# Performance work log

Measured on AMD Instinct MI355X. Metric: run time of the kernel, lower is better.

Reference implementation:

```python
import jax, jax.numpy as jnp
import numpy as np

N_NODES = 250000
N_EDGES = 4000000

def gcn_layer(x, src, dst, W, b, n_nodes):
    # PyG GCNConv: linear transform, add self-loops, symmetric normalization,
    # scatter-add aggregation at target nodes, then bias.
    xw = x @ W                                            # [N, out]
    deg = jax.ops.segment_sum(jnp.ones_like(src, dtype=xw.dtype), dst,
                              num_segments=n_nodes) + 1.0  # +1 for self loop
    dinv = deg ** -0.5                                     # deg >= 1 due to self loops
    norm = dinv[src] * dinv[dst]                           # [E]
    agg = jax.ops.segment_sum(norm[:, None] * xw[src], dst,
                              num_segments=n_nodes)        # neighbor messages
    out = agg + (dinv * dinv)[:, None] * xw + b            # self-loop message + bias
    return out


def setup_inputs() -> dict:
    key = jax.random.key(0)
    ks = jax.random.split(key, 8)
    x = jax.random.normal(ks[0], (N_NODES, 2), dtype=jnp.float32)
    edge_index = jax.random.randint(ks[1], (2, N_EDGES), 0, N_NODES, dtype=jnp.int64)
    def glorot(k, shape):
        lim = np.sqrt(6.0 / (shape[0] + shape[1]))
        return jax.random.uniform(k, shape, jnp.float32, -lim, lim)
    return {
        "x": x,
        "edge_index": edge_index,
        "W1": glorot(ks[2], (2, 16)),  "b1": jnp.zeros((16,), jnp.float32),
        "W2": glorot(ks[3], (16, 16)), "b2": jnp.zeros((16,), jnp.float32),
        "W3": glorot(ks[4], (16, 1)),  "b3": jnp.zeros((1,), jnp.float32),
    }


def reference(x, edge_index, W1, b1, W2, b2, W3, b3):
    src, dst = edge_index[0], edge_index[1]
    n = x.shape[0]
    h = jax.nn.relu(gcn_layer(x, src, dst, W1, b1, n))
    h = jax.nn.relu(gcn_layer(h, src, dst, W2, b2, n))
    return gcn_layer(h, src, dst, W3, b3, n)
```

## Files before the change

### kernel.cpp

```cpp
#include <hip/hip_runtime.h>


constexpr int K   = 977;
constexpr int NPW = 256;
constexpr int G   = 256;
constexpr int F   = 16;


__global__ __launch_bounds__(1024) void k_bcount(const int* __restrict__ dst,
        int* __restrict__ bcount, int E, int chunk) {
    __shared__ int h[K];
    for (int k = threadIdx.x; k < K; k += 1024) h[k] = 0;
    __syncthreads();
    int beg = blockIdx.x * chunk;
    int end = min(beg + chunk, E);
    for (int i = beg + threadIdx.x; i < end; i += 1024) {
        int d = __builtin_nontemporal_load(&dst[i]);
        atomicAdd(&h[d >> 8], 1);
    }
    __syncthreads();
    for (int k = threadIdx.x; k < K; k += 1024)
        bcount[blockIdx.x * K + k] = h[k];
}

__global__ __launch_bounds__(1024) void k_scan(int* __restrict__ bcount,
        int* __restrict__ colbase, int E) {
    __shared__ int tot[1024];
    int k = threadIdx.x;
    int s = 0;
    if (k < K) for (int b = 0; b < G; ++b) s += bcount[b * K + k];
    tot[k] = s;
    __syncthreads();
    for (int off = 1; off < 1024; off <<= 1) {
        int t = (k >= off) ? tot[k - off] : 0;
        __syncthreads();
        tot[k] += t;
        __syncthreads();
    }
    if (k < K) {
        int run = tot[k] - s;
        colbase[k] = run;
        for (int b = 0; b < G; ++b) {
            int t = bcount[b * K + k];
            bcount[b * K + k] = run;
            run += t;
        }
    }
    if (k == 0) colbase[K] = E;
}

__global__ __launch_bounds__(1024) void k_bfill(const int* __restrict__ src,
        const int* __restrict__ dst, const int* __restrict__ base,
        int* __restrict__ ent, int E, int chunk) {
    __shared__ int cur[K];
    for (int k = threadIdx.x; k < K; k += 1024)
        cur[k] = base[blockIdx.x * K + k];
    __syncthreads();
    int beg = blockIdx.x * chunk;
    int end = min(beg + chunk, E);
    for (int i = beg + threadIdx.x; i < end; i += 1024) {
        int d = __builtin_nontemporal_load(&dst[i]);
        int s = __builtin_nontemporal_load(&src[i]);
        int pos = atomicAdd(&cur[d >> 8], 1);
        ent[pos] = (s << 8) | (d & 255);
    }
}


__global__ __launch_bounds__(256) void k_prep(const int* __restrict__ ent,
        const int* __restrict__ colbase, const float* __restrict__ x,
        float* __restrict__ dinv, float* __restrict__ dx, int n) {
    __shared__ int h[NPW];
    h[threadIdx.x] = 0;
    __syncthreads();
    int beg = colbase[blockIdx.x], end = colbase[blockIdx.x + 1];
    for (int e = beg + threadIdx.x; e < end; e += 256) {
        int v = __builtin_nontemporal_load(&ent[e]);
        atomicAdd(&h[v & 255], 1);
    }
    __syncthreads();
    int i = (blockIdx.x << 8) + threadIdx.x;
    if (i < n) {
        float di = rsqrtf((float)h[threadIdx.x] + 1.0f);
        dinv[i] = di;
        float2 xv = reinterpret_cast<const float2*>(x)[i];
        reinterpret_cast<float2*>(dx)[i] = make_float2(di * xv.x, di * xv.y);
    }
}


__global__ __launch_bounds__(512) void k_layer1(const int* __restrict__ ent,
        const int* __restrict__ colbase, const float* __restrict__ dinv,
        const float* __restrict__ dx, const float* __restrict__ W1,
        const float* __restrict__ b1, float* __restrict__ dh1, int n) {
    __shared__ float acc[NPW * 2];
    __shared__ float sW[32];
    __shared__ float sb[16];
    if (threadIdx.x < 32) sW[threadIdx.x] = W1[threadIdx.x];
    if (threadIdx.x >= 32 && threadIdx.x < 48) sb[threadIdx.x - 32] = b1[threadIdx.x - 32];
    for (int t = threadIdx.x; t < NPW * 2; t += 512) acc[t] = 0.0f;
    __syncthreads();
    int beg = colbase[blockIdx.x], end = colbase[blockIdx.x + 1];
    int e = beg + threadIdx.x;
    for (; e + 512 < end; e += 1024) {
        int v0 = __builtin_nontemporal_load(&ent[e]);
        int v1 = __builtin_nontemporal_load(&ent[e + 512]);
        float2 a0 = reinterpret_cast<const float2*>(dx)[v0 >> 8];
        float2 a1 = reinterpret_cast<const float2*>(dx)[v1 >> 8];
        atomicAdd(&acc[(v0 & 255) * 2 + 0], a0.x);
        atomicAdd(&acc[(v0 & 255) * 2 + 1], a0.y);
        atomicAdd(&acc[(v1 & 255) * 2 + 0], a1.x);
        atomicAdd(&acc[(v1 & 255) * 2 + 1], a1.y);
    }
    if (e < end) {
        int v = __builtin_nontemporal_load(&ent[e]);
        float2 a = reinterpret_cast<const float2*>(dx)[v >> 8];
        atomicAdd(&acc[(v & 255) * 2 + 0], a.x);
        atomicAdd(&acc[(v & 255) * 2 + 1], a.y);
    }
    __syncthreads();
    int r = threadIdx.x;
    if (r < NPW) {
        int i = (blockIdx.x << 8) + r;
        if (i < n) {
            float di = dinv[i];
            float2 ds = reinterpret_cast<const float2*>(dx)[i];
            float a0 = di * (acc[r * 2 + 0] + ds.x);
            float a1 = di * (acc[r * 2 + 1] + ds.y);
            float4* orow = reinterpret_cast<float4*>(dh1 + (size_t)i * F);
#pragma unroll
            for (int q = 0; q < 4; ++q) {
                float4 o;
                o.x = di * fmaxf(a0 * sW[4*q+0] + a1 * sW[16 + 4*q+0] + sb[4*q+0], 0.0f);
                o.y = di * fmaxf(a0 * sW[4*q+1] + a1 * sW[16 + 4*q+1] + sb[4*q+1], 0.0f);
                o.z = di * fmaxf(a0 * sW[4*q+2] + a1 * sW[16 + 4*q+2] + sb[4*q+2], 0.0f);
                o.w = di * fmaxf(a0 * sW[4*q+3] + a1 * sW[16 + 4*q+3] + sb[4*q+3], 0.0f);
                orow[q] = o;
            }
        }
    }
}


__global__ __launch_bounds__(512) void k_layer2(const int* __restrict__ ent,
        const int* __restrict__ colbase, const float* __restrict__ dinv,
        const float* __restrict__ dh1, const float* __restrict__ W2,
        const float* __restrict__ b2, const float* __restrict__ W3,
        float* __restrict__ dxw3, int n) {
    __shared__ float acc[NPW * 17];
    __shared__ float sW2[256];
    __shared__ float sW3[16];
    __shared__ float sb[16];
    if (threadIdx.x < 256) sW2[threadIdx.x] = W2[threadIdx.x];
    if (threadIdx.x >= 256 && threadIdx.x < 272) sW3[threadIdx.x - 256] = W3[threadIdx.x - 256];
    if (threadIdx.x >= 272 && threadIdx.x < 288) sb[threadIdx.x - 272] = b2[threadIdx.x - 272];
    for (int t = threadIdx.x; t < NPW * 17; t += 512) acc[t] = 0.0f;
    __syncthreads();
    int beg = colbase[blockIdx.x], end = colbase[blockIdx.x + 1];
    int q4 = (threadIdx.x & 3) * 4;
    int eg = threadIdx.x >> 2;
    int e = beg + eg;
    for (; e + 128 < end; e += 256) {
        int v0 = __builtin_nontemporal_load(&ent[e]);
        int v1 = __builtin_nontemporal_load(&ent[e + 128]);
        float4 r0 = *reinterpret_cast<const float4*>(dh1 + (size_t)(v0 >> 8) * F + q4);
        float4 r1 = *reinterpret_cast<const float4*>(dh1 + (size_t)(v1 >> 8) * F + q4);
        int b0 = (v0 & 255) * 17 + q4;
        int b1_ = (v1 & 255) * 17 + q4;
        atomicAdd(&acc[b0 + 0], r0.x);
        atomicAdd(&acc[b0 + 1], r0.y);
        atomicAdd(&acc[b0 + 2], r0.z);
        atomicAdd(&acc[b0 + 3], r0.w);
        atomicAdd(&acc[b1_ + 0], r1.x);
        atomicAdd(&acc[b1_ + 1], r1.y);
        atomicAdd(&acc[b1_ + 2], r1.z);
        atomicAdd(&acc[b1_ + 3], r1.w);
    }
    if (e < end) {
        int v = __builtin_nontemporal_load(&ent[e]);
        float4 r = *reinterpret_cast<const float4*>(dh1 + (size_t)(v >> 8) * F + q4);
        int b0 = (v & 255) * 17 + q4;
        atomicAdd(&acc[b0 + 0], r.x);
        atomicAdd(&acc[b0 + 1], r.y);
        atomicAdd(&acc[b0 + 2], r.z);
        atomicAdd(&acc[b0 + 3], r.w);
    }
    __syncthreads();
    int r = threadIdx.x;
    if (r < NPW) {
        int i = (blockIdx.x << 8) + r;
        if (i < n) {
            float di = dinv[i];
            const float* dh = dh1 + (size_t)i * F;
            float a[16];
#pragma unroll
            for (int q = 0; q < 16; ++q) a[q] = di * (acc[r * 17 + q] + dh[q]);
            float sum = 0.0f;
#pragma unroll
            for (int c = 0; c < 16; ++c) {
                float h = sb[c];
#pragma unroll
                for (int q = 0; q < 16; ++q) h += a[q] * sW2[q * 16 + c];
                sum += fmaxf(h, 0.0f) * sW3[c];
            }
            dxw3[i] = di * sum;
        }
    }
}


__global__ __launch_bounds__(512) void k_out(const int* __restrict__ ent,
        const int* __restrict__ colbase, const float* __restrict__ dinv,
        const float* __restrict__ dxw3, const float* __restrict__ b3,
        float* __restrict__ out, int n) {
    __shared__ float acc[NPW];
    for (int t = threadIdx.x; t < NPW; t += 512) acc[t] = 0.0f;
    __syncthreads();
    int beg = colbase[blockIdx.x], end = colbase[blockIdx.x + 1];
    int e = beg + threadIdx.x;
    for (; e + 512 < end; e += 1024) {
        int v0 = __builtin_nontemporal_load(&ent[e]);
        int v1 = __builtin_nontemporal_load(&ent[e + 512]);
        float s0 = dxw3[v0 >> 8];
        float s1 = dxw3[v1 >> 8];
        atomicAdd(&acc[v0 & 255], s0);
        atomicAdd(&acc[v1 & 255], s1);
    }
    if (e < end) {
        int v = __builtin_nontemporal_load(&ent[e]);
        atomicAdd(&acc[v & 255], dxw3[v >> 8]);
    }
    __syncthreads();
    int r = threadIdx.x;
    if (r < NPW) {
        int i = (blockIdx.x << 8) + r;
        if (i < n) out[i] = dinv[i] * (acc[r] + dxw3[i]) + b3[0];
    }
}


extern "C" void kernel_launch(void* const* d_in, const int* in_sizes, int n_in,
                              void* d_out, int out_size, void* d_ws, size_t ws_size,
                              hipStream_t stream) {
    const float* x  = (const float*)d_in[0];
    const int*   ei = (const int*)d_in[1];
    const float* W1 = (const float*)d_in[2];
    const float* b1 = (const float*)d_in[3];
    const float* W2 = (const float*)d_in[4];
    const float* b2 = (const float*)d_in[5];
    const float* W3 = (const float*)d_in[6];
    const float* b3 = (const float*)d_in[7];

    const int n = in_sizes[0] / 2;
    const int E = in_sizes[1] / 2;
    const int* src = ei;
    const int* dst = ei + E;

    char* w = (char*)d_ws;
    int*   ent     = (int*)w;                    w += (size_t)E * 4;
    int*   bcount  = (int*)w;                    w += (size_t)G * K * 4;
    float* dinv    = (float*)w;                  w += (size_t)n * 4;
    float* dx      = (float*)w;                  w += (size_t)n * 2 * 4;
    float* dh1     = (float*)w;                  w += (size_t)n * F * 4;
    float* dxw3    = (float*)w;                  w += (size_t)n * 4;
    int*   colbase = (int*)w;                    w += (size_t)(K + 1) * 4;
    float* out     = (float*)d_out;

    const int chunk = (E + G - 1) / G;

    k_bcount<<<G, 1024, 0, stream>>>(dst, bcount, E, chunk);
    k_scan  <<<1, 1024, 0, stream>>>(bcount, colbase, E);
    k_bfill <<<G, 1024, 0, stream>>>(src, dst, bcount, ent, E, chunk);

    k_prep<<<K, 256, 0, stream>>>(ent, colbase, x, dinv, dx, n);

    k_layer1<<<K, 512, 0, stream>>>(ent, colbase, dinv, dx, W1, b1, dh1, n);
    k_layer2<<<K, 512, 0, stream>>>(ent, colbase, dinv, dh1, W2, b2, W3, dxw3, n);
    k_out   <<<K, 512, 0, stream>>>(ent, colbase, dinv, dxw3, b3, out, n);
}
```

Before: 544.1 us.

## Pre-sort edges by source tile before destination bucketing; retune layer2 block size

Adds a first counting-sort pass that groups edges by source-node tile (8192 nodes), packing dst and the source offset into one word held in a buffer aliased over the node-feature pool. The destination bucket fill then runs over source-ordered edges, so within each destination bucket the source ids come out roughly sorted. The aim is better cache locality for the dh1/dx gathers in the layer kernels. This costs an extra full pass over the edge list plus scan kernels. Layer2 separately drops to 256 threads with a 4-way unrolled gather loop.

```diff
diff --git a/kernel.cpp b/kernel.cpp
--- a/kernel.cpp
+++ b/kernel.cpp
@@ -1,13 +1,74 @@
 #include <hip/hip_runtime.h>
 
 
-constexpr int K   = 977;
-constexpr int NPW = 256;
-constexpr int G   = 256;
-constexpr int F   = 16;
-
-
-__global__ __launch_bounds__(1024) void k_bcount(const int* __restrict__ dst,
+constexpr int K    = 977;
+constexpr int NPW  = 256;
+constexpr int G    = 256;
+constexpr int F    = 16;
+constexpr int TILE = 8192;
+constexpr int TMAX = 64;
+
+
+__global__ __launch_bounds__(1024) void k_acount(const int* __restrict__ src,
+        int* __restrict__ acount, int E, int chunk, int T) {
+    __shared__ int h[TMAX];
+    if (threadIdx.x < TMAX) h[threadIdx.x] = 0;
+    __syncthreads();
+    int beg = blockIdx.x * chunk;
+    int end = min(beg + chunk, E);
+    for (int i = beg + threadIdx.x; i < end; i += 1024) {
+        int s = __builtin_nontemporal_load(&src[i]);
+        atomicAdd(&h[s / TILE], 1);
+    }
+    __syncthreads();
+    if (threadIdx.x < T) acount[blockIdx.x * T + threadIdx.x] = h[threadIdx.x];
+}
+
+__global__ __launch_bounds__(256) void k_ascan(int* __restrict__ acount,
+        int* __restrict__ tbase, int E, int T) {
+    __shared__ int tot[TMAX];
+    int t = threadIdx.x;
+    if (t < T) {
+        int s = 0;
+        for (int b = 0; b < G; ++b) s += acount[b * T + t];
+        tot[t] = s;
+    }
+    __syncthreads();
+    if (t == 0) {
+        int run = 0;
+        for (int q = 0; q < T; ++q) { int c = tot[q]; tot[q] = run; run += c; }
+    }
+    __syncthreads();
+    if (t < T) {
+        int run = tot[t];
+        tbase[t] = run;
+        for (int b = 0; b < G; ++b) {
+            int c = acount[b * T + t];
+            acount[b * T + t] = run;
+            run += c;
+        }
+    }
+    if (t == 0) tbase[T] = E;
+}
+
+__global__ __launch_bounds__(1024) void k_afill(const int* __restrict__ src,
+        const int* __restrict__ dst, const int* __restrict__ abase,
+        unsigned int* __restrict__ entA, int E, int chunk, int T) {
+    __shared__ int cur[TMAX];
+    if (threadIdx.x < T) cur[threadIdx.x] = abase[blockIdx.x * T + threadIdx.x];
+    __syncthreads();
+    int beg = blockIdx.x * chunk;
+    int end = min(beg + chunk, E);
+    for (int i = beg + threadIdx.x; i < end; i += 1024) {
+        int s = __builtin_nontemporal_load(&src[i]);
+        int d = __builtin_nontemporal_load(&dst[i]);
+        int pos = atomicAdd(&cur[s / TILE], 1);
+        entA[pos] = ((unsigned int)d << 13) | (unsigned int)(s & (TILE - 1));
+    }
+}
+
+
+__global__ __launch_bounds__(1024) void k_bcount(const unsigned int* __restrict__ entA,
         int* __restrict__ bcount, int E, int chunk) {
     __shared__ int h[K];
     for (int k = threadIdx.x; k < K; k += 1024) h[k] = 0;
@@ -15,8 +76,8 @@
     int beg = blockIdx.x * chunk;
     int end = min(beg + chunk, E);
     for (int i = beg + threadIdx.x; i < end; i += 1024) {
-        int d = __builtin_nontemporal_load(&dst[i]);
-        atomicAdd(&h[d >> 8], 1);
+        unsigned int v = __builtin_nontemporal_load(&entA[i]);
+        atomicAdd(&h[(v >> 13) >> 8], 1);
     }
     __syncthreads();
     for (int k = threadIdx.x; k < K; k += 1024)
@@ -49,18 +110,23 @@
     if (k == 0) colbase[K] = E;
 }
 
-__global__ __launch_bounds__(1024) void k_bfill(const int* __restrict__ src,
-        const int* __restrict__ dst, const int* __restrict__ base,
-        int* __restrict__ ent, int E, int chunk) {
+__global__ __launch_bounds__(1024) void k_bfill(const unsigned int* __restrict__ entA,
+        const int* __restrict__ tbase, const int* __restrict__ base,
+        int* __restrict__ ent, int E, int chunk, int T) {
     __shared__ int cur[K];
+    __shared__ int tb[TMAX + 1];
     for (int k = threadIdx.x; k < K; k += 1024)
         cur[k] = base[blockIdx.x * K + k];
+    if (threadIdx.x <= T) tb[threadIdx.x] = tbase[threadIdx.x];
     __syncthreads();
     int beg = blockIdx.x * chunk;
     int end = min(beg + chunk, E);
+    int t = 0;
     for (int i = beg + threadIdx.x; i < end; i += 1024) {
-        int d = __builtin_nontemporal_load(&dst[i]);
-        int s = __builtin_nontemporal_load(&src[i]);
+        while (i >= tb[t + 1]) ++t;
+        unsigned int v = __builtin_nontemporal_load(&entA[i]);
+        int d = (int)(v >> 13);
+        int s = (t * TILE) + (int)(v & (TILE - 1));
         int pos = atomicAdd(&cur[d >> 8], 1);
         ent[pos] = (s << 8) | (d & 255);
     }
@@ -142,7 +208,7 @@
 }
 
 
-__global__ __launch_bounds__(512) void k_layer2(const int* __restrict__ ent,
+__global__ __launch_bounds__(256) void k_layer2(const int* __restrict__ ent,
         const int* __restrict__ colbase, const float* __restrict__ dinv,
         const float* __restrict__ dh1, const float* __restrict__ W2,
         const float* __restrict__ b2, const float* __restrict__ W3,
@@ -151,43 +217,48 @@
     __shared__ float sW2[256];
     __shared__ float sW3[16];
     __shared__ float sb[16];
-    if (threadIdx.x < 256) sW2[threadIdx.x] = W2[threadIdx.x];
-    if (threadIdx.x >= 256 && threadIdx.x < 272) sW3[threadIdx.x - 256] = W3[threadIdx.x - 256];
-    if (threadIdx.x >= 272 && threadIdx.x < 288) sb[threadIdx.x - 272] = b2[threadIdx.x - 272];
-    for (int t = threadIdx.x; t < NPW * 17; t += 512) acc[t] = 0.0f;
+    int tid = threadIdx.x;
+    sW2[tid] = W2[tid];
+    if (tid < 16) sW3[tid] = W3[tid];
+    else if (tid < 32) sb[tid - 16] = b2[tid - 16];
+    for (int t = tid; t < NPW * 17; t += 256) acc[t] = 0.0f;
     __syncthreads();
     int beg = colbase[blockIdx.x], end = colbase[blockIdx.x + 1];
-    int q4 = (threadIdx.x & 3) * 4;
-    int eg = threadIdx.x >> 2;
+    int q4 = (tid & 3) * 4;
+    int eg = tid >> 2;
     int e = beg + eg;
-    for (; e + 128 < end; e += 256) {
+    for (; e + 192 < end; e += 256) {
         int v0 = __builtin_nontemporal_load(&ent[e]);
-        int v1 = __builtin_nontemporal_load(&ent[e + 128]);
+        int v1 = __builtin_nontemporal_load(&ent[e + 64]);
+        int v2 = __builtin_nontemporal_load(&ent[e + 128]);
+        int v3 = __builtin_nontemporal_load(&ent[e + 192]);
         float4 r0 = *reinterpret_cast<const float4*>(dh1 + (size_t)(v0 >> 8) * F + q4);
         float4 r1 = *reinterpret_cast<const float4*>(dh1 + (size_t)(v1 >> 8) * F + q4);
+        float4 r2 = *reinterpret_cast<const float4*>(dh1 + (size_t)(v2 >> 8) * F + q4);
+        float4 r3 = *reinterpret_cast<const float4*>(dh1 + (size_t)(v3 >> 8) * F + q4);
         int b0 = (v0 & 255) * 17 + q4;
         int b1_ = (v1 & 255) * 17 + q4;
-        atomicAdd(&acc[b0 + 0], r0.x);
-        atomicAdd(&acc[b0 + 1], r0.y);
-        atomicAdd(&acc[b0 + 2], r0.z);
-        atomicAdd(&acc[b0 + 3], r0.w);
-        atomicAdd(&acc[b1_ + 0], r1.x);
-        atomicAdd(&acc[b1_ + 1], r1.y);
-        atomicAdd(&acc[b1_ + 2], r1.z);
-        atomicAdd(&acc[b1_ + 3], r1.w);
-    }
-    if (e < end) {
+        int b2_ = (v2 & 255) * 17 + q4;
+        int b3_ = (v3 & 255) * 17 + q4;
+        atomicAdd(&acc[b0 + 0], r0.x); atomicAdd(&acc[b0 + 1], r0.y);
+        atomicAdd(&acc[b0 + 2], r0.z); atomicAdd(&acc[b0 + 3], r0.w);
+        atomicAdd(&acc[b1_ + 0], r1.x); atomicAdd(&acc[b1_ + 1], r1.y);
+        atomicAdd(&acc[b1_ + 2], r1.z); atomicAdd(&acc[b1_ + 3], r1.w);
+        atomicAdd(&acc[b2_ + 0], r2.x); atomicAdd(&acc[b2_ + 1], r2.y);
+        atomicAdd(&acc[b2_ + 2], r2.z); atomicAdd(&acc[b2_ + 3], r2.w);
+        atomicAdd(&acc[b3_ + 0], r3.x); atomicAdd(&acc[b3_ + 1], r3.y);
+        atomicAdd(&acc[b3_ + 2], r3.z); atomicAdd(&acc[b3_ + 3], r3.w);
+    }
+    for (; e < end; e += 64) {
         int v = __builtin_nontemporal_load(&ent[e]);
         float4 r = *reinterpret_cast<const float4*>(dh1 + (size_t)(v >> 8) * F + q4);
         int b0 = (v & 255) * 17 + q4;
-        atomicAdd(&acc[b0 + 0], r.x);
-        atomicAdd(&acc[b0 + 1], r.y);
-        atomicAdd(&acc[b0 + 2], r.z);
-        atomicAdd(&acc[b0 + 3], r.w);
-    }
-    __syncthreads();
-    int r = threadIdx.x;
-    if (r < NPW) {
+        atomicAdd(&acc[b0 + 0], r.x); atomicAdd(&acc[b0 + 1], r.y);
+        atomicAdd(&acc[b0 + 2], r.z); atomicAdd(&acc[b0 + 3], r.w);
+    }
+    __syncthreads();
+    int r = tid;
+    {
         int i = (blockIdx.x << 8) + r;
         if (i < n) {
             float di = dinv[i];
@@ -255,26 +326,36 @@
     const int E = in_sizes[1] / 2;
     const int* src = ei;
     const int* dst = ei + E;
+    const int T = (n + TILE - 1) / TILE;
 
     char* w = (char*)d_ws;
     int*   ent     = (int*)w;                    w += (size_t)E * 4;
     int*   bcount  = (int*)w;                    w += (size_t)G * K * 4;
-    float* dinv    = (float*)w;                  w += (size_t)n * 4;
-    float* dx      = (float*)w;                  w += (size_t)n * 2 * 4;
-    float* dh1     = (float*)w;                  w += (size_t)n * F * 4;
-    float* dxw3    = (float*)w;                  w += (size_t)n * 4;
+    int*   acount  = (int*)w;                    w += (size_t)G * TMAX * 4;
     int*   colbase = (int*)w;                    w += (size_t)(K + 1) * 4;
+    int*   tbase   = (int*)w;                    w += (size_t)(TMAX + 1) * 4;
+    w = (char*)(((uintptr_t)w + 15) & ~(uintptr_t)15);
+    char* pool = w;
+    unsigned int* entA = (unsigned int*)pool;
+    float* dinv    = (float*)pool;               pool += (size_t)n * 4;
+    float* dx      = (float*)pool;               pool += (size_t)n * 2 * 4;
+    float* dh1     = (float*)pool;               pool += (size_t)n * F * 4;
+    float* dxw3    = (float*)pool;               pool += (size_t)n * 4;
     float* out     = (float*)d_out;
 
     const int chunk = (E + G - 1) / G;
 
-    k_bcount<<<G, 1024, 0, stream>>>(dst, bcount, E, chunk);
+    k_acount<<<G, 1024, 0, stream>>>(src, acount, E, chunk, T);
+    k_ascan <<<1, 256, 0, stream>>>(acount, tbase, E, T);
+    k_afill <<<G, 1024, 0, stream>>>(src, dst, acount, entA, E, chunk, T);
+
+    k_bcount<<<G, 1024, 0, stream>>>(entA, bcount, E, chunk);
     k_scan  <<<1, 1024, 0, stream>>>(bcount, colbase, E);
-    k_bfill <<<G, 1024, 0, stream>>>(src, dst, bcount, ent, E, chunk);
+    k_bfill <<<G, 1024, 0, stream>>>(entA, tbase, bcount, ent, E, chunk, T);
 
     k_prep<<<K, 256, 0, stream>>>(ent, colbase, x, dinv, dx, n);
 
     k_layer1<<<K, 512, 0, stream>>>(ent, colbase, dinv, dx, W1, b1, dh1, n);
-    k_layer2<<<K, 512, 0, stream>>>(ent, colbase, dinv, dh1, W2, b2, W3, dxw3, n);
+    k_layer2<<<K, 256, 0, stream>>>(ent, colbase, dinv, dh1, W2, b2, W3, dxw3, n);
     k_out   <<<K, 512, 0, stream>>>(ent, colbase, dinv, dxw3, b3, out, n);
 }
```

New measurement: 584.2 us. 1.07x slower.
